# Kernel tuning notes

Hardware: AMD Instinct MI355X
Metric: run time of the kernel (lower is better)

## Reference

```python
import jax, jax.numpy as jnp
import numpy as np
from jax import lax

N_NODES = 100000
N_EDGES = 1600000
FEAT = 8          # per-node feature dim
STATE = 4         # embed_dim
OUT = 16          # n classes
HID = 5           # hardcoded state_l1/output_l1
MAX_IT = 10


def setup_inputs() -> dict:
    key = jax.random.key(0)
    ks = jax.random.split(key, 12)
    edge_parent = jax.random.randint(ks[0], (N_EDGES,), 0, N_NODES, dtype=jnp.int32)
    edge_child = jax.random.randint(ks[1], (N_EDGES,), 0, N_NODES, dtype=jnp.int32)
    # arc_feat = inp[:, 1:] = [child_id, feat_parent, feat_child]  -> [E, 1+2F]
    feats = jax.random.normal(ks[2], (N_EDGES, 2 * FEAT), jnp.float32)
    arc_feat = jnp.concatenate([edge_child.astype(jnp.float32)[:, None], feats], axis=1)
    d_in = 1 + 2 * FEAT + STATE  # Net.state_input = input_dim - 1 + state_dim = 21
    std = 0.1  # truncated_normal(stddev=0.1) init in original
    W1 = std * jax.random.normal(ks[3], (d_in, HID), jnp.float32)
    b1 = jnp.zeros((HID,), jnp.float32)
    W2 = std * jax.random.normal(ks[4], (HID, STATE), jnp.float32)
    b2 = jnp.zeros((STATE,), jnp.float32)
    Wo1 = std * jax.random.normal(ks[5], (STATE, HID), jnp.float32)
    bo1 = jnp.zeros((HID,), jnp.float32)
    Wo2 = std * jax.random.normal(ks[6], (HID, OUT), jnp.float32)
    bo2 = jnp.zeros((OUT,), jnp.float32)
    return {
        'arc_feat': arc_feat, 'W1': W1, 'b1': b1, 'W2': W2, 'b2': b2,
        'Wo1': Wo1, 'bo1': bo1, 'Wo2': Wo2, 'bo2': bo2,
        'edge_parent': edge_parent, 'edge_child': edge_child,
        'n_nodes': N_NODES, 'max_it': MAX_IT,
    }


def reference(arc_feat, W1, b1, W2, b2, Wo1, bo1, Wo2, bo2,
              edge_parent, edge_child, n_nodes, max_it):
    state_dim = W2.shape[1]

    def step(state, _):
        gat = state[edge_child]                                  # [E, S] gather neighbor state
        x = jnp.concatenate([arc_feat, gat], axis=1)             # [E, D-1+S]
        h = jnp.tanh(x @ W1 + b1)                                # netSt layer1 [E, 5]
        m = jnp.tanh(h @ W2 + b2)                                # netSt layer2 [E, S]
        # sparse ArcNode @ m  == segment-sum edge messages to parent node
        new_state = jax.ops.segment_sum(m, edge_parent, num_segments=n_nodes)
        return new_state, None

    state0 = jnp.zeros((n_nodes, state_dim), arc_feat.dtype)
    state, _ = lax.scan(step, state0, None, length=max_it)       # fixed max_it iterations
    # netOut: node-based output (graph_based=False)
    ho = jnp.tanh(state @ Wo1 + bo1)                             # [N, 5]
    out = jax.nn.softmax(ho @ Wo2 + bo2, axis=-1)                # [N, OUT]
    return out
```

## Files before the change

### kernel.cpp

```cpp
#include <hip/hip_runtime.h>

#define N_NODES 100000
#define N_EDGES 1600000
#define STATE 4
#define OUT_C 16
#define HID 5
#define MAX_IT 10
#define ARC_D 17

__device__ __forceinline__ float fast_tanh(float x) {
    float e = __expf(2.0f * x);
    return 1.0f - 2.0f / (e + 1.0f);
}

__global__ void hist_kernel(const int* __restrict__ parent, int* __restrict__ counts, int E) {
    int e = blockIdx.x * blockDim.x + threadIdx.x;
    if (e < E) atomicAdd(&counts[parent[e]], 1);
}

#define SCAN_B 1024
__global__ __launch_bounds__(SCAN_B) void scanA(const int* __restrict__ counts,
                                                int* __restrict__ off,
                                                int* __restrict__ bsum, int n) {
    __shared__ int lds[SCAN_B];
    int t = threadIdx.x;
    int i = blockIdx.x * SCAN_B + t;
    int v = (i < n - 1) ? counts[i] : 0;
    lds[t] = v;
    for (int s = 1; s < SCAN_B; s <<= 1) {
        __syncthreads();
        int u = (t >= s) ? lds[t - s] : 0;
        __syncthreads();
        lds[t] += u;
    }
    __syncthreads();
    if (i < n) off[i] = lds[t] - v;
    if (t == SCAN_B - 1) bsum[blockIdx.x] = lds[t];
}

__global__ __launch_bounds__(128) void scanB(int* __restrict__ bsum, int nb) {
    __shared__ int lds[128];
    int t = threadIdx.x;
    int v = (t < nb) ? bsum[t] : 0;
    lds[t] = v;
    for (int s = 1; s < 128; s <<= 1) {
        __syncthreads();
        int u = (t >= s) ? lds[t - s] : 0;
        __syncthreads();
        lds[t] += u;
    }
    __syncthreads();
    if (t < nb) bsum[t] = lds[t] - v;
}

__global__ __launch_bounds__(SCAN_B) void scanC(int* __restrict__ off, const int* __restrict__ bsum,
                                                int* __restrict__ cursor, int n) {
    int i = blockIdx.x * SCAN_B + threadIdx.x;
    if (i < n) {
        int v = off[i] + bsum[blockIdx.x];
        off[i] = v;
        if (i < n - 1) cursor[i] = v;
    }
}

#define BBLK 256
__global__ __launch_bounds__(BBLK) void build_kernel(const float* __restrict__ arc,
                                                     const float* __restrict__ W1,
                                                     const float* __restrict__ b1,
                                                     const int* __restrict__ parent,
                                                     const int* __restrict__ child,
                                                     int* __restrict__ cursor,
                                                     float4* __restrict__ rec, int E) {
    __shared__ float lds[BBLK * ARC_D];
    int t = threadIdx.x;
    int base = blockIdx.x * BBLK;
    int cnt = E - base; if (cnt > BBLK) cnt = BBLK;
    for (int k = t; k < cnt * ARC_D; k += BBLK)
        lds[k] = arc[(size_t)base * ARC_D + k];
    __syncthreads();
    if (t < cnt) {
        int e = base + t;
        const float* row = &lds[t * ARC_D];
        float p[HID];
        #pragma unroll
        for (int j = 0; j < HID; ++j) p[j] = b1[j];
        #pragma unroll
        for (int i = 0; i < ARC_D; ++i) {
            float x = row[i];
            #pragma unroll
            for (int j = 0; j < HID; ++j) p[j] += x * W1[i * HID + j];
        }
        int pa = parent[e];
        int pos = atomicAdd(&cursor[pa], 1);
        rec[2 * (size_t)pos]     = make_float4(p[0], p[1], p[2], p[3]);
        rec[2 * (size_t)pos + 1] = make_float4(p[4], __uint_as_float((unsigned)child[e]),
                                               __uint_as_float((unsigned)pa), 0.0f);
    }
}

__global__ __launch_bounds__(256) void iter_kernel(const float4* __restrict__ rec,
                                                   const float* __restrict__ W1,
                                                   const float* __restrict__ W2,
                                                   const float* __restrict__ b2,
                                                   const float* __restrict__ src,
                                                   float* __restrict__ dst, int E) {
    int e = blockIdx.x * blockDim.x + threadIdx.x;
    int lane = threadIdx.x & 63;
    float w1b[STATE][HID];
    #pragma unroll
    for (int k = 0; k < STATE; ++k)
        #pragma unroll
        for (int j = 0; j < HID; ++j) w1b[k][j] = W1[(ARC_D + k) * HID + j];
    float w2[HID][STATE];
    #pragma unroll
    for (int j = 0; j < HID; ++j)
        #pragma unroll
        for (int k = 0; k < STATE; ++k) w2[j][k] = W2[j * STATE + k];
    float b2v[STATE];
    #pragma unroll
    for (int k = 0; k < STATE; ++k) b2v[k] = b2[k];

    float m0 = 0.f, m1 = 0.f, m2 = 0.f, m3 = 0.f;
    int p = -1;
    if (e < E) {
        float4 r0 = rec[2 * (size_t)e];
        float4 r1 = rec[2 * (size_t)e + 1];
        int c = (int)__float_as_uint(r1.y);
        p = (int)__float_as_uint(r1.z);
        float4 s = ((const float4*)src)[c];
        float pr[HID] = {r0.x, r0.y, r0.z, r0.w};
        pr[4] = r1.x;
        float h[HID];
        #pragma unroll
        for (int j = 0; j < HID; ++j) {
            float v = pr[j] + s.x * w1b[0][j] + s.y * w1b[1][j]
                            + s.z * w1b[2][j] + s.w * w1b[3][j];
            h[j] = fast_tanh(v);
        }
        float mm[STATE];
        #pragma unroll
        for (int k = 0; k < STATE; ++k) {
            float v = b2v[k];
            #pragma unroll
            for (int j = 0; j < HID; ++j) v += h[j] * w2[j][k];
            mm[k] = fast_tanh(v);
        }
        m0 = mm[0]; m1 = mm[1]; m2 = mm[2]; m3 = mm[3];
    }
    #pragma unroll
    for (int d = 1; d < 64; d <<= 1) {
        int   pp = __shfl_up(p, d);
        float t0 = __shfl_up(m0, d);
        float t1 = __shfl_up(m1, d);
        float t2 = __shfl_up(m2, d);
        float t3 = __shfl_up(m3, d);
        bool ok = (lane >= d) && (pp == p);
        if (ok) { m0 += t0; m1 += t1; m2 += t2; m3 += t3; }
    }
    int pn = __shfl_down(p, 1);
    bool tail = (lane == 63) || (pn != p);
    if (tail && e < E) {
        float* d4 = &dst[(size_t)p * STATE];
        atomicAdd(&d4[0], m0);
        atomicAdd(&d4[1], m1);
        atomicAdd(&d4[2], m2);
        atomicAdd(&d4[3], m3);
    }
}

__global__ __launch_bounds__(256) void out_kernel(const float* __restrict__ state,
                                                  const float* __restrict__ Wo1,
                                                  const float* __restrict__ bo1,
                                                  const float* __restrict__ Wo2,
                                                  const float* __restrict__ bo2,
                                                  float* __restrict__ out) {
    int n = blockIdx.x * blockDim.x + threadIdx.x;
    if (n >= N_NODES) return;
    float4 s = ((const float4*)state)[n];
    float ho[HID];
    #pragma unroll
    for (int j = 0; j < HID; ++j) {
        float v = bo1[j] + s.x * Wo1[0 * HID + j] + s.y * Wo1[1 * HID + j]
                         + s.z * Wo1[2 * HID + j] + s.w * Wo1[3 * HID + j];
        ho[j] = fast_tanh(v);
    }
    float lg[OUT_C];
    float mx = -1e30f;
    #pragma unroll
    for (int o = 0; o < OUT_C; ++o) {
        float v = bo2[o];
        #pragma unroll
        for (int j = 0; j < HID; ++j) v += ho[j] * Wo2[j * OUT_C + o];
        lg[o] = v; mx = fmaxf(mx, v);
    }
    float sum = 0.f;
    #pragma unroll
    for (int o = 0; o < OUT_C; ++o) { lg[o] = __expf(lg[o] - mx); sum += lg[o]; }
    float inv = 1.0f / sum;
    float4* op = (float4*)&out[(size_t)n * OUT_C];
    op[0] = make_float4(lg[0] * inv, lg[1] * inv, lg[2] * inv, lg[3] * inv);
    op[1] = make_float4(lg[4] * inv, lg[5] * inv, lg[6] * inv, lg[7] * inv);
    op[2] = make_float4(lg[8] * inv, lg[9] * inv, lg[10] * inv, lg[11] * inv);
    op[3] = make_float4(lg[12] * inv, lg[13] * inv, lg[14] * inv, lg[15] * inv);
}

extern "C" void kernel_launch(void* const* d_in, const int* in_sizes, int n_in,
                              void* d_out, int out_size, void* d_ws, size_t ws_size,
                              hipStream_t stream) {
    const float* arc   = (const float*)d_in[0];
    const float* W1    = (const float*)d_in[1];
    const float* b1    = (const float*)d_in[2];
    const float* W2    = (const float*)d_in[3];
    const float* b2    = (const float*)d_in[4];
    const float* Wo1   = (const float*)d_in[5];
    const float* bo1   = (const float*)d_in[6];
    const float* Wo2   = (const float*)d_in[7];
    const float* bo2   = (const float*)d_in[8];
    const int* parent  = (const int*)d_in[9];
    const int* child   = (const int*)d_in[10];
    float* out = (float*)d_out;

    char* ws = (char*)d_ws;
    size_t o = 0;
    auto alloc = [&](size_t bytes) { void* p = ws + o; o += (bytes + 255) & ~255ULL; return p; };
    float4* rec   = (float4*)alloc((size_t)N_EDGES * 32);
    float* states = (float*)alloc((size_t)(MAX_IT + 1) * N_NODES * STATE * 4);
    int*   counts = (int*)alloc((size_t)N_NODES * 4);
    int*   off    = (int*)alloc((size_t)(N_NODES + 1) * 4);
    int*   cursor = (int*)alloc((size_t)N_NODES * 4);
    int*   bsum   = (int*)alloc(1024 * 4);

    hipMemsetAsync(counts, 0, (size_t)N_NODES * 4, stream);
    hipMemsetAsync(states, 0, (size_t)(MAX_IT + 1) * N_NODES * STATE * 4, stream);

    hist_kernel<<<(N_EDGES + 255) / 256, 256, 0, stream>>>(parent, counts, N_EDGES);
    int n = N_NODES + 1;
    int nb = (n + SCAN_B - 1) / SCAN_B;
    scanA<<<nb, SCAN_B, 0, stream>>>(counts, off, bsum, n);
    scanB<<<1, 128, 0, stream>>>(bsum, nb);
    scanC<<<nb, SCAN_B, 0, stream>>>(off, bsum, cursor, n);
    build_kernel<<<(N_EDGES + BBLK - 1) / BBLK, BBLK, 0, stream>>>(arc, W1, b1, parent, child,
                                                                   cursor, rec, N_EDGES);
    for (int it = 0; it < MAX_IT; ++it) {
        const float* src = states + (size_t)it * N_NODES * STATE;
        float* dst = states + (size_t)(it + 1) * N_NODES * STATE;
        iter_kernel<<<(N_EDGES + 255) / 256, 256, 0, stream>>>(rec, W1, W2, b2, src, dst, N_EDGES);
    }
    out_kernel<<<(N_NODES + 255) / 256, 256, 0, stream>>>(
        states + (size_t)MAX_IT * N_NODES * STATE, Wo1, bo1, Wo2, bo2, out);
}
```

Baseline: 525.8 us.

## Write edge records coalesced then permute; replace atomics with plain stores when segment fits in wave

The build kernel now writes per-edge records in natural (coalesced) order and records a permutation, and a new kernel gathers them into parent-sorted order, replacing scattered 32-byte writes. In the iteration kernel, a node whose entire edge segment lies within one wavefront now gets its sum written with a single float4 store instead of four atomics. This adds an extra 51 MB buffer and a permute pass, plus two extra off[] loads per segment tail in each iteration.

Measured after the change: 717.7 us. +36.5%, slower.

```diff
diff --git a/kernel.cpp b/kernel.cpp
--- a/kernel.cpp
+++ b/kernel.cpp
@@ -64,13 +64,14 @@
 }
 
 #define BBLK 256
-__global__ __launch_bounds__(BBLK) void build_kernel(const float* __restrict__ arc,
-                                                     const float* __restrict__ W1,
-                                                     const float* __restrict__ b1,
-                                                     const int* __restrict__ parent,
-                                                     const int* __restrict__ child,
-                                                     int* __restrict__ cursor,
-                                                     float4* __restrict__ rec, int E) {
+__global__ __launch_bounds__(BBLK) void build_nat(const float* __restrict__ arc,
+                                                  const float* __restrict__ W1,
+                                                  const float* __restrict__ b1,
+                                                  const int* __restrict__ parent,
+                                                  const int* __restrict__ child,
+                                                  int* __restrict__ cursor,
+                                                  float4* __restrict__ rec_nat,
+                                                  int* __restrict__ perm, int E) {
     __shared__ float lds[BBLK * ARC_D];
     int t = threadIdx.x;
     int base = blockIdx.x * BBLK;
@@ -91,14 +92,28 @@
             for (int j = 0; j < HID; ++j) p[j] += x * W1[i * HID + j];
         }
         int pa = parent[e];
+        rec_nat[2 * (size_t)e]     = make_float4(p[0], p[1], p[2], p[3]);
+        rec_nat[2 * (size_t)e + 1] = make_float4(p[4], __uint_as_float((unsigned)child[e]),
+                                                 __uint_as_float((unsigned)pa), 0.0f);
         int pos = atomicAdd(&cursor[pa], 1);
-        rec[2 * (size_t)pos]     = make_float4(p[0], p[1], p[2], p[3]);
-        rec[2 * (size_t)pos + 1] = make_float4(p[4], __uint_as_float((unsigned)child[e]),
-                                               __uint_as_float((unsigned)pa), 0.0f);
-    }
+        perm[pos] = e;
+    }
+}
+
+__global__ __launch_bounds__(256) void permute_rec(const int* __restrict__ perm,
+                                                   const float4* __restrict__ rec_nat,
+                                                   float4* __restrict__ rec, int E) {
+    int i = blockIdx.x * blockDim.x + threadIdx.x;
+    if (i >= E) return;
+    int e = perm[i];
+    float4 a = rec_nat[2 * (size_t)e];
+    float4 b = rec_nat[2 * (size_t)e + 1];
+    rec[2 * (size_t)i]     = a;
+    rec[2 * (size_t)i + 1] = b;
 }
 
 __global__ __launch_bounds__(256) void iter_kernel(const float4* __restrict__ rec,
+                                                   const int* __restrict__ off,
                                                    const float* __restrict__ W1,
                                                    const float* __restrict__ W2,
                                                    const float* __restrict__ b2,
@@ -160,11 +175,17 @@
     int pn = __shfl_down(p, 1);
     bool tail = (lane == 63) || (pn != p);
     if (tail && e < E) {
-        float* d4 = &dst[(size_t)p * STATE];
-        atomicAdd(&d4[0], m0);
-        atomicAdd(&d4[1], m1);
-        atomicAdd(&d4[2], m2);
-        atomicAdd(&d4[3], m3);
+        int wbase = blockIdx.x * blockDim.x + (threadIdx.x & ~63);
+        int g0 = off[p], g1 = off[p + 1];
+        if (g0 >= wbase && g1 <= wbase + 64) {
+            ((float4*)dst)[p] = make_float4(m0, m1, m2, m3);
+        } else {
+            float* d4 = &dst[(size_t)p * STATE];
+            atomicAdd(&d4[0], m0);
+            atomicAdd(&d4[1], m1);
+            atomicAdd(&d4[2], m2);
+            atomicAdd(&d4[3], m3);
+        }
     }
 }
 
@@ -223,12 +244,14 @@
     char* ws = (char*)d_ws;
     size_t o = 0;
     auto alloc = [&](size_t bytes) { void* p = ws + o; o += (bytes + 255) & ~255ULL; return p; };
-    float4* rec   = (float4*)alloc((size_t)N_EDGES * 32);
-    float* states = (float*)alloc((size_t)(MAX_IT + 1) * N_NODES * STATE * 4);
-    int*   counts = (int*)alloc((size_t)N_NODES * 4);
-    int*   off    = (int*)alloc((size_t)(N_NODES + 1) * 4);
-    int*   cursor = (int*)alloc((size_t)N_NODES * 4);
-    int*   bsum   = (int*)alloc(1024 * 4);
+    float4* rec     = (float4*)alloc((size_t)N_EDGES * 32);
+    float4* rec_nat = (float4*)alloc((size_t)N_EDGES * 32);
+    float*  states  = (float*)alloc((size_t)(MAX_IT + 1) * N_NODES * STATE * 4);
+    int*    perm    = (int*)alloc((size_t)N_EDGES * 4);
+    int*    counts  = (int*)alloc((size_t)N_NODES * 4);
+    int*    off     = (int*)alloc((size_t)(N_NODES + 1) * 4);
+    int*    cursor  = (int*)alloc((size_t)N_NODES * 4);
+    int*    bsum    = (int*)alloc(1024 * 4);
 
     hipMemsetAsync(counts, 0, (size_t)N_NODES * 4, stream);
     hipMemsetAsync(states, 0, (size_t)(MAX_IT + 1) * N_NODES * STATE * 4, stream);
@@ -239,12 +262,13 @@
     scanA<<<nb, SCAN_B, 0, stream>>>(counts, off, bsum, n);
     scanB<<<1, 128, 0, stream>>>(bsum, nb);
     scanC<<<nb, SCAN_B, 0, stream>>>(off, bsum, cursor, n);
-    build_kernel<<<(N_EDGES + BBLK - 1) / BBLK, BBLK, 0, stream>>>(arc, W1, b1, parent, child,
-                                                                   cursor, rec, N_EDGES);
+    build_nat<<<(N_EDGES + BBLK - 1) / BBLK, BBLK, 0, stream>>>(arc, W1, b1, parent, child,
+                                                                cursor, rec_nat, perm, N_EDGES);
+    permute_rec<<<(N_EDGES + 255) / 256, 256, 0, stream>>>(perm, rec_nat, rec, N_EDGES);
     for (int it = 0; it < MAX_IT; ++it) {
         const float* src = states + (size_t)it * N_NODES * STATE;
         float* dst = states + (size_t)(it + 1) * N_NODES * STATE;
-        iter_kernel<<<(N_EDGES + 255) / 256, 256, 0, stream>>>(rec, W1, W2, b2, src, dst, N_EDGES);
+        iter_kernel<<<(N_EDGES + 255) / 256, 256, 0, stream>>>(rec, off, W1, W2, b2, src, dst, N_EDGES);
     }
     out_kernel<<<(N_NODES + 255) / 256, 256, 0, stream>>>(
         states + (size_t)MAX_IT * N_NODES * STATE, Wo1, bo1, Wo2, bo2, out);
```
